# Performance work log

Measured on AMD Instinct MI355X. Metric: run time of the kernel, lower is better.

## Reference

```python
import jax, jax.numpy as jnp
import numpy as np

N = 100000   # nodes
E = 1600000  # edges
G = 64       # graphs in batch
DIMS = [(7, 128), (128, 128), (128, 256)]
EPS = 1e-5


def setup_inputs() -> dict:
    key = jax.random.key(0)
    ks = jax.random.split(key, 32)
    inp = {}
    inp["x"] = jax.random.normal(ks[0], (N, 7), dtype=jnp.float32)
    inp["edge_index"] = jax.random.randint(ks[1], (2, E), 0, N, dtype=jnp.int64)
    inp["batch"] = jnp.sort(jax.random.randint(ks[2], (N,), 0, G, dtype=jnp.int64))
    ki = 3
    for i, (din, dout) in enumerate(DIMS):
        inp[f"Wl{i}"] = jax.random.normal(ks[ki], (din, dout), dtype=jnp.float32) * 0.05; ki += 1
        inp[f"bl{i}"] = jnp.zeros((dout,), dtype=jnp.float32)
        inp[f"Wr{i}"] = jax.random.normal(ks[ki], (din, dout), dtype=jnp.float32) * 0.05; ki += 1
        inp[f"g{i}"] = jax.random.uniform(ks[ki], (dout,), dtype=jnp.float32) + 0.5; ki += 1
        inp[f"be{i}"] = jax.random.normal(ks[ki], (dout,), dtype=jnp.float32) * 0.1; ki += 1
        inp[f"rm{i}"] = jax.random.normal(ks[ki], (dout,), dtype=jnp.float32) * 0.1; ki += 1
        inp[f"rv{i}"] = jax.random.uniform(ks[ki], (dout,), dtype=jnp.float32) + 0.5; ki += 1
    return inp


def _sage(x, src, dst, Wl, bl, Wr):
    # mean-aggregate neighbor features: out[i] = mean_{(j->i)} x[j]
    agg = jax.ops.segment_sum(x[src], dst, num_segments=N)          # [N, din]
    cnt = jax.ops.segment_sum(jnp.ones((src.shape[0],), x.dtype), dst, num_segments=N)
    mean = agg / jnp.maximum(cnt, 1.0)[:, None]
    return x @ Wl + bl + mean @ Wr


def _bn_relu(x, g, be, rm, rv):
    # BatchNorm1d in eval mode (running stats) + ReLU; dropout is a no-op in eval
    return jax.nn.relu((x - rm) * jax.lax.rsqrt(rv + EPS) * g + be)


def reference(x, edge_index, batch,
              Wl0, bl0, Wr0, g0, be0, rm0, rv0,
              Wl1, bl1, Wr1, g1, be1, rm1, rv1,
              Wl2, bl2, Wr2, g2, be2, rm2, rv2):
    src, dst = edge_index[0], edge_index[1]
    layers = [(Wl0, bl0, Wr0, g0, be0, rm0, rv0),
              (Wl1, bl1, Wr1, g1, be1, rm1, rv1),
              (Wl2, bl2, Wr2, g2, be2, rm2, rv2)]
    for Wl, bl, Wr, g, be, rm, rv in layers:
        x = _sage(x, src, dst, Wl, bl, Wr)
        x = _bn_relu(x, g, be, rm, rv)
    pooled = jax.ops.segment_sum(x, batch, num_segments=G)  # global_add_pool
    return (pooled, x)
```

## Files before the change

### kernel.cpp

```cpp
#include <hip/hip_runtime.h>
#include <hip/hip_bf16.h>

#define EPSV 1e-5f
#define PSHIFT 6
#define PMASK 63
#define PCAP 1536
#define B1SHIFT 11
#define B1MASK ((1 << B1SHIFT) - 1)
#define B1CAP 34816
#define SPLIT 16

typedef __attribute__((ext_vector_type(8))) short bf16x8;
typedef __attribute__((ext_vector_type(4))) float f32x4;
typedef __attribute__((ext_vector_type(4))) unsigned u32x4;

__device__ __forceinline__ float bf2f(unsigned short u) {
    unsigned x = ((unsigned)u) << 16;
    return __builtin_bit_cast(float, x);
}
__device__ __forceinline__ unsigned short f2bf(float f) {
    unsigned x = __builtin_bit_cast(unsigned, f);
    unsigned r = (x + 0x7fffu + ((x >> 16) & 1u)) >> 16;
    return (unsigned short)r;
}
__device__ __forceinline__ f32x4 bflo4(u32x4 v) {
    f32x4 r;
    r.x = __builtin_bit_cast(float, v.x << 16);
    r.y = __builtin_bit_cast(float, v.y << 16);
    r.z = __builtin_bit_cast(float, v.z << 16);
    r.w = __builtin_bit_cast(float, v.w << 16);
    return r;
}
__device__ __forceinline__ f32x4 bfhi4(u32x4 v) {
    f32x4 r;
    r.x = __builtin_bit_cast(float, v.x & 0xffff0000u);
    r.y = __builtin_bit_cast(float, v.y & 0xffff0000u);
    r.z = __builtin_bit_cast(float, v.z & 0xffff0000u);
    r.w = __builtin_bit_cast(float, v.w & 0xffff0000u);
    return r;
}


__global__ __launch_bounds__(256) void k_scatter1(const int* __restrict__ src,
                                                  const int* __restrict__ dst,
                                                  int* __restrict__ bcnt1,
                                                  unsigned* __restrict__ stg1,
                                                  int E, int NB1) {
    __shared__ int hist[64], sbase[64], scur[64];
    int t = threadIdx.x;
    int base = blockIdx.x * 2048;
    if (t < 64) { hist[t] = 0; scur[t] = 0; }
    __syncthreads();
    unsigned val[8];
    int cb[8];
#pragma unroll
    for (int k = 0; k < 8; k++) {
        int i = base + k * 256 + t;
        if (i < E) {
            int d = __builtin_nontemporal_load(&dst[i]);
            int s = __builtin_nontemporal_load(&src[i]);
            cb[k] = d >> B1SHIFT;
            val[k] = ((unsigned)s << B1SHIFT) | (unsigned)(d & B1MASK);
            atomicAdd(&hist[cb[k]], 1);
        } else
            cb[k] = -1;
    }
    __syncthreads();
    if (t < NB1 && hist[t] > 0) sbase[t] = atomicAdd(&bcnt1[t], hist[t]);
    __syncthreads();
#pragma unroll
    for (int k = 0; k < 8; k++) {
        if (cb[k] >= 0) {
            int r = atomicAdd(&scur[cb[k]], 1);
            int slot = sbase[cb[k]] + r;
            if (slot < B1CAP) stg1[(size_t)cb[k] * B1CAP + slot] = val[k];
        }
    }
}

__global__ __launch_bounds__(256) void k_scatter2(const int* __restrict__ bcnt1,
                                                  const unsigned* __restrict__ stg1,
                                                  int* __restrict__ pcnt,
                                                  unsigned* __restrict__ pstg) {
    __shared__ int hist[32], sbase[32], scur[32];
    int cb = blockIdx.x >> 4;
    int sl = blockIdx.x & (SPLIT - 1);
    int t = threadIdx.x;
    if (t < 32) { hist[t] = 0; scur[t] = 0; }
    int cnt = min(bcnt1[cb], B1CAP);
    int per = (cnt + SPLIT - 1) / SPLIT;
    int lo = sl * per, hi = min(lo + per, cnt);
    __syncthreads();
    const unsigned* sp = stg1 + (size_t)cb * B1CAP;
    for (int j = lo + t; j < hi; j += 256)
        atomicAdd(&hist[(sp[j] >> 6) & 31], 1);
    __syncthreads();
    if (t < 32 && hist[t] > 0) sbase[t] = atomicAdd(&pcnt[(cb << 5) + t], hist[t]);
    __syncthreads();
    for (int j = lo + t; j < hi; j += 256) {
        unsigned v = sp[j];
        int pr = (v >> 6) & 31;
        int r = atomicAdd(&scur[pr], 1);
        int slot = sbase[pr] + r;
        if (slot < PCAP)
            pstg[(size_t)((cb << 5) + pr) * PCAP + slot] =
                ((v >> 5) & ~63u) | (v & 63u);
    }
}

__global__ __launch_bounds__(256) void k_meta(const int* __restrict__ pcnt,
                                              int* __restrict__ pbase,
                                              int* __restrict__ off,
                                              const int* __restrict__ batch,
                                              int* __restrict__ gstart,
                                              int NPART, int Nn, int G) {
    if (blockIdx.x == 1) {
        int g = threadIdx.x;
        if (g > G) return;
        if (g == G) {
            gstart[G] = Nn;
            return;
        }
        int lo = 0, hi = Nn;
        while (lo < hi) {
            int mid = (lo + hi) >> 1;
            if (batch[mid] < g) lo = mid + 1;
            else hi = mid;
        }
        gstart[g] = lo;
        return;
    }
    __shared__ int red[256];
    int t = threadIdx.x;
    int chunk = (NPART + 255) / 256;
    int lo = t * chunk, hi = min(lo + chunk, NPART);
    int s = 0;
    for (int p = lo; p < hi; p++) {
        int tt = min(pcnt[p], PCAP);
        pbase[p] = tt;
        s += tt;
    }
    red[t] = s;
    __syncthreads();
    for (int d = 1; d < 256; d <<= 1) {
        int v = (t >= d) ? red[t - d] : 0;
        __syncthreads();
        red[t] += v;
        __syncthreads();
    }
    int base = (t == 0) ? 0 : red[t - 1];
    for (int p = lo; p < hi; p++) {
        int tt = pbase[p];
        pbase[p] = base;
        base += tt;
    }
    if (t == 255) off[Nn] = red[255];
}

__global__ __launch_bounds__(256) void k_build(const int* __restrict__ pcnt,
                                               const unsigned* __restrict__ pstg,
                                               const int* __restrict__ pbase,
                                               int* __restrict__ off,
                                               int* __restrict__ csr, int Nn) {
    __shared__ unsigned ed[PCAP];
    __shared__ int srt[PCAP];
    __shared__ int cnt[64], loff[64], cur[64];
    int p = blockIdx.x, t = threadIdx.x;
    int tot = min(pcnt[p], PCAP);
    if (t < 64) cnt[t] = 0;
    __syncthreads();
    const unsigned* sp = pstg + (size_t)p * PCAP;
    for (int j = t; j < tot; j += 256) {
        unsigned e = __builtin_nontemporal_load(&sp[j]);
        ed[j] = e;
        atomicAdd(&cnt[e & PMASK], 1);
    }
    __syncthreads();
    if (t == 0) {
        int a = 0;
        for (int j = 0; j < 64; j++) {
            loff[j] = a;
            cur[j] = a;
            a += cnt[j];
        }
    }
    __syncthreads();
    int base = pbase[p];
    int node0 = p << PSHIFT;
    if (t < 64 && node0 + t < Nn) off[node0 + t] = base + loff[t];
    for (int j = t; j < tot; j += 256) {
        unsigned e = ed[j];
        int pos = atomicAdd(&cur[e & PMASK], 1);
        srt[pos] = (int)(e >> PSHIFT);
    }
    __syncthreads();
    for (int j = t; j < tot; j += 256) csr[base + j] = srt[j];
}


__global__ __launch_bounds__(256) void k_agg7(const float* __restrict__ x,
                                              const int* __restrict__ off,
                                              const int* __restrict__ csr,
                                              float* __restrict__ mean, int n) {
    int i = (blockIdx.x * 256 + threadIdx.x) >> 3;
    int r = threadIdx.x & 7;
    if (i >= n) return;
    int a = off[i], b = off[i + 1];
    float acc = 0.f;
    if (r < 7) {
        int j = a;
        for (; j + 1 < b; j += 2)
            acc += x[(size_t)csr[j] * 7 + r] + x[(size_t)csr[j + 1] * 7 + r];
        if (j < b) acc += x[(size_t)csr[j] * 7 + r];
    }
    float inv = 1.0f / (float)max(b - a, 1);
    if (r < 7) mean[(size_t)i * 7 + r] = acc * inv;
}

__global__ __launch_bounds__(256) void k_agg128(const unsigned short* __restrict__ x,
                                                const int* __restrict__ off,
                                                const int* __restrict__ csr,
                                                unsigned short* __restrict__ mean,
                                                int n) {
    int q = (blockIdx.x * 256 + threadIdx.x) >> 4;
    int sl = threadIdx.x & 15;
    if (q >= n) return;
    int a = off[q], b = off[q + 1];
    const u32x4* xr = (const u32x4*)x;
    f32x4 aL = {0.f, 0.f, 0.f, 0.f}, aH = {0.f, 0.f, 0.f, 0.f};
    int j = a;
    for (; j + 7 < b; j += 8) {
        u32x4 v[8];
#pragma unroll
        for (int t = 0; t < 8; t++) {
            int s = __builtin_nontemporal_load(&csr[j + t]);
            v[t] = xr[(size_t)s * 16 + sl];
        }
#pragma unroll
        for (int t = 0; t < 8; t++) {
            aL += bflo4(v[t]);
            aH += bfhi4(v[t]);
        }
    }
    for (; j + 3 < b; j += 4) {
        u32x4 v[4];
#pragma unroll
        for (int t = 0; t < 4; t++) {
            int s = __builtin_nontemporal_load(&csr[j + t]);
            v[t] = xr[(size_t)s * 16 + sl];
        }
#pragma unroll
        for (int t = 0; t < 4; t++) {
            aL += bflo4(v[t]);
            aH += bfhi4(v[t]);
        }
    }
    for (; j < b; j++) {
        int s = __builtin_nontemporal_load(&csr[j]);
        u32x4 v = xr[(size_t)s * 16 + sl];
        aL += bflo4(v);
        aH += bfhi4(v);
    }
    float inv = 1.0f / (float)max(b - a, 1);
    u32x4 o;
    o.x = (unsigned)f2bf(aL.x * inv) | ((unsigned)f2bf(aH.x * inv) << 16);
    o.y = (unsigned)f2bf(aL.y * inv) | ((unsigned)f2bf(aH.y * inv) << 16);
    o.z = (unsigned)f2bf(aL.z * inv) | ((unsigned)f2bf(aH.z * inv) << 16);
    o.w = (unsigned)f2bf(aL.w * inv) | ((unsigned)f2bf(aH.w * inv) << 16);
    *((u32x4*)mean + (size_t)q * 16 + sl) = o;
}


__global__ __launch_bounds__(256) void k_prepw_all(
    const float* __restrict__ Wl1, const float* __restrict__ Wr1,
    const float* __restrict__ Wl2, const float* __restrict__ Wr2,
    unsigned short* __restrict__ Wlt1, unsigned short* __restrict__ Wrt1,
    unsigned short* __restrict__ Wlt2, unsigned short* __restrict__ Wrt2) {
    int u = blockIdx.x * 256 + threadIdx.x;
    const float* W;
    unsigned short* Wt;
    int Ncols, v;
    if (u < 32768) {
        v = u & 16383;
        W = (u < 16384) ? Wl1 : Wr1;
        Wt = (u < 16384) ? Wlt1 : Wrt1;
        Ncols = 128;
    } else {
        v = (u - 32768) & 32767;
        W = (u < 65536) ? Wl2 : Wr2;
        Wt = (u < 65536) ? Wlt2 : Wrt2;
        Ncols = 256;
    }
    int n = v % Ncols, k = v / Ncols;
    Wt[(size_t)n * 128 + k] = f2bf(W[(size_t)k * Ncols + n]);
}


__global__ __launch_bounds__(256) void k_layer0(
    const float* __restrict__ x, const float* __restrict__ mean,
    const float* __restrict__ Wl, const float* __restrict__ bl,
    const float* __restrict__ Wr, const float* __restrict__ g,
    const float* __restrict__ be, const float* __restrict__ rm,
    const float* __restrict__ rv, unsigned short* __restrict__ out, int n) {
    int tid = threadIdx.x;
    int col = tid & 127;
    int r = tid >> 7;
    int row = blockIdx.x * 2 + r;
    if (row >= n) return;
    float sc = g[col] * rsqrtf(rv[col] + EPSV);
    float sh = (bl[col] - rm[col]) * sc + be[col];
    const float* xp = x + (size_t)row * 7;
    const float* mp = mean + (size_t)row * 7;
    float acc = 0.f;
#pragma unroll
    for (int k = 0; k < 7; k++) acc += xp[k] * Wl[k * 128 + col];
#pragma unroll
    for (int k = 0; k < 7; k++) acc += mp[k] * Wr[k * 128 + col];
    float h = acc * sc + sh;
    out[(size_t)row * 128 + col] = f2bf(fmaxf(h, 0.f));
}


template <int COLS, int DOUT, bool BF16OUT>
__global__ __launch_bounds__(256) void k_mfma_layer(
    const unsigned short* __restrict__ xin, const unsigned short* __restrict__ meanb,
    const unsigned short* __restrict__ Wlt, const unsigned short* __restrict__ Wrt,
    const float* __restrict__ bl, const float* __restrict__ g,
    const float* __restrict__ be, const float* __restrict__ rm,
    const float* __restrict__ rv, void* __restrict__ outv, int n) {
    __shared__ unsigned short As[64 * 40];
    __shared__ unsigned short Bs[COLS * 40];

    int tid = threadIdx.x;
    int wave = tid >> 6;
    int lane = tid & 63;
    int m = lane & 15;
    int half = lane >> 4;
    int row0 = blockIdx.x * 64;
    int colbase = blockIdx.y * COLS;

    const int NCB = COLS / 16;
    f32x4 acc[NCB] = {};

    for (int s = 0; s < 8; s++) {
        int pass = s >> 2;
        int k0 = (s & 3) * 32;
        const unsigned short* Asrc = pass ? meanb : xin;
        const unsigned short* Wt = pass ? Wrt : Wlt;

        __syncthreads();
        {
            int rr = tid >> 2;
            int ks = (tid & 3) * 8;
            int grow = row0 + rr;
            float4 v = make_float4(0.f, 0.f, 0.f, 0.f);
            if (grow < n) v = *(const float4*)&Asrc[(size_t)grow * 128 + k0 + ks];
            *(float4*)&As[rr * 40 + ks] = v;
        }
#pragma unroll
        for (int rep = 0; rep < COLS / 64; rep++) {
            int u = tid + rep * 256;
            int nn = u >> 2;
            int ks = (u & 3) * 8;
            float4 v = *(const float4*)&Wt[(size_t)(colbase + nn) * 128 + k0 + ks];
            *(float4*)&Bs[nn * 40 + ks] = v;
        }
        __syncthreads();

        bf16x8 a = *(const bf16x8*)&As[(wave * 16 + m) * 40 + half * 8];
#pragma unroll
        for (int cb = 0; cb < NCB; cb++) {
            bf16x8 b = *(const bf16x8*)&Bs[(cb * 16 + m) * 40 + half * 8];
            acc[cb] = __builtin_amdgcn_mfma_f32_16x16x32_bf16(a, b, acc[cb], 0, 0, 0);
        }
    }

    float* outf = (float*)outv;
    unsigned short* outb = (unsigned short*)outv;
#pragma unroll
    for (int cb = 0; cb < NCB; cb++) {
        int col = colbase + cb * 16 + m;
        float sc = g[col] * rsqrtf(rv[col] + EPSV);
        float sh = (bl[col] - rm[col]) * sc + be[col];
#pragma unroll
        for (int reg = 0; reg < 4; reg++) {
            int r0 = row0 + wave * 16 + half * 4 + reg;
            if (r0 < n) {
                float h = fmaxf(acc[cb][reg] * sc + sh, 0.f);
                if (BF16OUT) outb[(size_t)r0 * DOUT + col] = f2bf(h);
                else outf[(size_t)r0 * DOUT + col] = h;
            }
        }
    }
}


__global__ __launch_bounds__(256) void k_pool(const float* __restrict__ x3,
                                              const int* __restrict__ gstart,
                                              float* __restrict__ pooled, int G) {
    const int S = 16;
    int g = blockIdx.x / S;
    int s = blockIdx.x % S;
    int a = gstart[g], b = gstart[g + 1];
    int col = threadIdx.x;
    float acc = 0.f;
    for (int r = a + s; r < b; r += S) acc += x3[(size_t)r * 256 + col];
    atomicAdd(&pooled[g * 256 + col], acc);
}


extern "C" void kernel_launch(void* const* d_in, const int* in_sizes, int n_in,
                              void* d_out, int out_size, void* d_ws, size_t ws_size,
                              hipStream_t stream) {
    const float* x = (const float*)d_in[0];
    const int* ei = (const int*)d_in[1];
    const int* batch = (const int*)d_in[2];
    const int N = in_sizes[0] / 7;
    const int E = in_sizes[1] / 2;
    const int G = 64;
    const int* src = ei;
    const int* dst = ei + E;
    const int NPART = (N + PMASK) >> PSHIFT;
    const int NB1 = (N + (1 << B1SHIFT) - 1) >> B1SHIFT;

    const float* P[21];
    for (int i = 0; i < 21; i++) P[i] = (const float*)d_in[3 + i];
    const float **L0 = P, **L1 = P + 7, **L2 = P + 14;

    char* w = (char*)d_ws;
    auto carve = [&](size_t bytes) {
        void* p = (void*)w;
        w += (bytes + 255) & ~(size_t)255;
        return p;
    };
    int* cnts = (int*)carve((size_t)(64 + NPART) * 4);
    int* bcnt1 = cnts;
    int* pcnt = cnts + 64;
    unsigned* stg1 = (unsigned*)carve((size_t)NB1 * B1CAP * 4);
    unsigned* pstg = (unsigned*)carve((size_t)NPART * PCAP * 4);
    int* pbase = (int*)carve((size_t)NPART * 4);
    int* off = (int*)carve(((size_t)N + 1) * 4);
    int* gstart = (int*)carve(((size_t)G + 1) * 4);
    float* mean7 = (float*)carve((size_t)N * 7 * 4);
    unsigned short* x1 = (unsigned short*)carve((size_t)N * 128 * 2);
    unsigned short* meanb = (unsigned short*)carve((size_t)N * 128 * 2);
    unsigned short* Wlt1 = (unsigned short*)carve((size_t)128 * 128 * 2);
    unsigned short* Wrt1 = (unsigned short*)carve((size_t)128 * 128 * 2);
    unsigned short* Wlt2 = (unsigned short*)carve((size_t)128 * 256 * 2);
    unsigned short* Wrt2 = (unsigned short*)carve((size_t)128 * 256 * 2);
    int* csr = (int*)stg1;

    float* pooled = (float*)d_out;
    float* x3 = (float*)d_out + (size_t)G * 256;

    hipMemsetAsync(cnts, 0, (size_t)(64 + NPART) * 4, stream);
    hipMemsetAsync(pooled, 0, (size_t)G * 256 * 4, stream);

    k_scatter1<<<(E + 2047) / 2048, 256, 0, stream>>>(src, dst, bcnt1, stg1, E, NB1);
    k_scatter2<<<NB1 * SPLIT, 256, 0, stream>>>(bcnt1, stg1, pcnt, pstg);
    k_meta<<<2, 256, 0, stream>>>(pcnt, pbase, off, batch, gstart, NPART, N, G);
    k_build<<<NPART, 256, 0, stream>>>(pcnt, pstg, pbase, off, csr, N);
    k_prepw_all<<<(98304 + 255) / 256, 256, 0, stream>>>(L1[0], L1[2], L2[0], L2[2],
                                                         Wlt1, Wrt1, Wlt2, Wrt2);

    k_agg7<<<(N * 8 + 255) / 256, 256, 0, stream>>>(x, off, csr, mean7, N);
    k_layer0<<<(N + 1) / 2, 256, 0, stream>>>(x, mean7, L0[0], L0[1], L0[2], L0[3],
                                              L0[4], L0[5], L0[6], x1, N);

    k_agg128<<<((size_t)N * 16 + 255) / 256, 256, 0, stream>>>(x1, off, csr, meanb, N);
    k_mfma_layer<128, 128, true><<<dim3((N + 63) / 64, 1), 256, 0, stream>>>(
        x1, meanb, Wlt1, Wrt1, L1[1], L1[3], L1[4], L1[5], L1[6], x1, N);

    k_agg128<<<((size_t)N * 16 + 255) / 256, 256, 0, stream>>>(x1, off, csr, meanb, N);
    k_mfma_layer<128, 256, false><<<dim3((N + 63) / 64, 2), 256, 0, stream>>>(
        x1, meanb, Wlt2, Wrt2, L2[1], L2[3], L2[4], L2[5], L2[6], x3, N);

    k_pool<<<G * 16, 256, 0, stream>>>(x3, gstart, pooled, G);
}
```

Baseline: 490.9 us.

## Fuse neighbor mean aggregation into MFMA layer kernels via shared memory

Removes the separate k_agg128 kernels and computes each 64-row tile's neighbor mean directly into shared memory inside the MFMA layer kernel, so the mean matrix is never written to and re-read from global memory. Layer 2 now computes all 256 output columns in a single block instead of splitting across two blocks on grid y, which avoids aggregating twice. The costs are more shared memory per block (lower occupancy), a less unrolled gather loop with fewer loads in flight, and a serial gather phase ahead of the GEMM that limits latency hiding. The output also moves from in-place x1 to a separate x2 buffer.

After: 498.8 us. About the same (+1.6%).

```diff
diff --git a/kernel.cpp b/kernel.cpp
--- a/kernel.cpp
+++ b/kernel.cpp
@@ -215,59 +215,6 @@
     }
     float inv = 1.0f / (float)max(b - a, 1);
     if (r < 7) mean[(size_t)i * 7 + r] = acc * inv;
-}
-
-__global__ __launch_bounds__(256) void k_agg128(const unsigned short* __restrict__ x,
-                                                const int* __restrict__ off,
-                                                const int* __restrict__ csr,
-                                                unsigned short* __restrict__ mean,
-                                                int n) {
-    int q = (blockIdx.x * 256 + threadIdx.x) >> 4;
-    int sl = threadIdx.x & 15;
-    if (q >= n) return;
-    int a = off[q], b = off[q + 1];
-    const u32x4* xr = (const u32x4*)x;
-    f32x4 aL = {0.f, 0.f, 0.f, 0.f}, aH = {0.f, 0.f, 0.f, 0.f};
-    int j = a;
-    for (; j + 7 < b; j += 8) {
-        u32x4 v[8];
-#pragma unroll
-        for (int t = 0; t < 8; t++) {
-            int s = __builtin_nontemporal_load(&csr[j + t]);
-            v[t] = xr[(size_t)s * 16 + sl];
-        }
-#pragma unroll
-        for (int t = 0; t < 8; t++) {
-            aL += bflo4(v[t]);
-            aH += bfhi4(v[t]);
-        }
-    }
-    for (; j + 3 < b; j += 4) {
-        u32x4 v[4];
-#pragma unroll
-        for (int t = 0; t < 4; t++) {
-            int s = __builtin_nontemporal_load(&csr[j + t]);
-            v[t] = xr[(size_t)s * 16 + sl];
-        }
-#pragma unroll
-        for (int t = 0; t < 4; t++) {
-            aL += bflo4(v[t]);
-            aH += bfhi4(v[t]);
-        }
-    }
-    for (; j < b; j++) {
-        int s = __builtin_nontemporal_load(&csr[j]);
-        u32x4 v = xr[(size_t)s * 16 + sl];
-        aL += bflo4(v);
-        aH += bfhi4(v);
-    }
-    float inv = 1.0f / (float)max(b - a, 1);
-    u32x4 o;
-    o.x = (unsigned)f2bf(aL.x * inv) | ((unsigned)f2bf(aH.x * inv) << 16);
-    o.y = (unsigned)f2bf(aL.y * inv) | ((unsigned)f2bf(aH.y * inv) << 16);
-    o.z = (unsigned)f2bf(aL.z * inv) | ((unsigned)f2bf(aH.z * inv) << 16);
-    o.w = (unsigned)f2bf(aL.w * inv) | ((unsigned)f2bf(aH.w * inv) << 16);
-    *((u32x4*)mean + (size_t)q * 16 + sl) = o;
 }
 
 
@@ -321,13 +268,15 @@
 }
 
 
-template <int COLS, int DOUT, bool BF16OUT>
-__global__ __launch_bounds__(256) void k_mfma_layer(
-    const unsigned short* __restrict__ xin, const unsigned short* __restrict__ meanb,
+template <int COLS, bool BF16OUT>
+__global__ __launch_bounds__(256) void k_fused_layer(
+    const unsigned short* __restrict__ xin,
+    const int* __restrict__ off, const int* __restrict__ csr,
     const unsigned short* __restrict__ Wlt, const unsigned short* __restrict__ Wrt,
     const float* __restrict__ bl, const float* __restrict__ g,
     const float* __restrict__ be, const float* __restrict__ rm,
     const float* __restrict__ rv, void* __restrict__ outv, int n) {
+    __shared__ unsigned short Ms[64 * 136];
     __shared__ unsigned short As[64 * 40];
     __shared__ unsigned short Bs[COLS * 40];
 
@@ -337,37 +286,76 @@
     int m = lane & 15;
     int half = lane >> 4;
     int row0 = blockIdx.x * 64;
-    int colbase = blockIdx.y * COLS;
+
+    {
+        int qw = tid >> 4;
+        int sl = tid & 15;
+        const u32x4* xr = (const u32x4*)xin;
+        for (int r4 = 0; r4 < 4; r4++) {
+            int row = qw * 4 + r4;
+            int grow = row0 + row;
+            f32x4 aL = {0.f, 0.f, 0.f, 0.f}, aH = {0.f, 0.f, 0.f, 0.f};
+            float inv = 0.f;
+            if (grow < n) {
+                int a = off[grow], b = off[grow + 1];
+                int j = a;
+                for (; j + 3 < b; j += 4) {
+                    int s0 = csr[j], s1 = csr[j + 1], s2 = csr[j + 2], s3 = csr[j + 3];
+                    u32x4 v0 = xr[(size_t)s0 * 16 + sl];
+                    u32x4 v1 = xr[(size_t)s1 * 16 + sl];
+                    u32x4 v2 = xr[(size_t)s2 * 16 + sl];
+                    u32x4 v3 = xr[(size_t)s3 * 16 + sl];
+                    aL += bflo4(v0) + bflo4(v1) + bflo4(v2) + bflo4(v3);
+                    aH += bfhi4(v0) + bfhi4(v1) + bfhi4(v2) + bfhi4(v3);
+                }
+                for (; j < b; j++) {
+                    u32x4 v = xr[(size_t)csr[j] * 16 + sl];
+                    aL += bflo4(v);
+                    aH += bfhi4(v);
+                }
+                inv = 1.0f / (float)max(b - a, 1);
+            }
+            u32x4 o;
+            o.x = (unsigned)f2bf(aL.x * inv) | ((unsigned)f2bf(aH.x * inv) << 16);
+            o.y = (unsigned)f2bf(aL.y * inv) | ((unsigned)f2bf(aH.y * inv) << 16);
+            o.z = (unsigned)f2bf(aL.z * inv) | ((unsigned)f2bf(aH.z * inv) << 16);
+            o.w = (unsigned)f2bf(aL.w * inv) | ((unsigned)f2bf(aH.w * inv) << 16);
+            *(u32x4*)&Ms[row * 136 + sl * 8] = o;
+        }
+    }
 
     const int NCB = COLS / 16;
     f32x4 acc[NCB] = {};
+    int rr = tid >> 2;
+    int ks = (tid & 3) * 8;
 
     for (int s = 0; s < 8; s++) {
         int pass = s >> 2;
         int k0 = (s & 3) * 32;
-        const unsigned short* Asrc = pass ? meanb : xin;
         const unsigned short* Wt = pass ? Wrt : Wlt;
 
         __syncthreads();
-        {
-            int rr = tid >> 2;
-            int ks = (tid & 3) * 8;
+        if (pass == 0) {
             int grow = row0 + rr;
             float4 v = make_float4(0.f, 0.f, 0.f, 0.f);
-            if (grow < n) v = *(const float4*)&Asrc[(size_t)grow * 128 + k0 + ks];
+            if (grow < n) v = *(const float4*)&xin[(size_t)grow * 128 + k0 + ks];
             *(float4*)&As[rr * 40 + ks] = v;
         }
 #pragma unroll
         for (int rep = 0; rep < COLS / 64; rep++) {
             int u = tid + rep * 256;
             int nn = u >> 2;
-            int ks = (u & 3) * 8;
-            float4 v = *(const float4*)&Wt[(size_t)(colbase + nn) * 128 + k0 + ks];
-            *(float4*)&Bs[nn * 40 + ks] = v;
+            int ks2 = (u & 3) * 8;
+            float4 v = *(const float4*)&Wt[(size_t)nn * 128 + k0 + ks2];
+            *(float4*)&Bs[nn * 40 + ks2] = v;
         }
         __syncthreads();
 
-        bf16x8 a = *(const bf16x8*)&As[(wave * 16 + m) * 40 + half * 8];
+        bf16x8 a;
+        if (pass == 0)
+            a = *(const bf16x8*)&As[(wave * 16 + m) * 40 + half * 8];
+        else
+            a = *(const bf16x8*)&Ms[(wave * 16 + m) * 136 + k0 + half * 8];
 #pragma unroll
         for (int cb = 0; cb < NCB; cb++) {
             bf16x8 b = *(const bf16x8*)&Bs[(cb * 16 + m) * 40 + half * 8];
@@ -379,7 +367,7 @@
     unsigned short* outb = (unsigned short*)outv;
 #pragma unroll
     for (int cb = 0; cb < NCB; cb++) {
-        int col = colbase + cb * 16 + m;
+        int col = cb * 16 + m;
         float sc = g[col] * rsqrtf(rv[col] + EPSV);
         float sh = (bl[col] - rm[col]) * sc + be[col];
 #pragma unroll
@@ -387,8 +375,8 @@
             int r0 = row0 + wave * 16 + half * 4 + reg;
             if (r0 < n) {
                 float h = fmaxf(acc[cb][reg] * sc + sh, 0.f);
-                if (BF16OUT) outb[(size_t)r0 * DOUT + col] = f2bf(h);
-                else outf[(size_t)r0 * DOUT + col] = h;
+                if (BF16OUT) outb[(size_t)r0 * COLS + col] = f2bf(h);
+                else outf[(size_t)r0 * COLS + col] = h;
             }
         }
     }
@@ -443,7 +431,7 @@
     int* gstart = (int*)carve(((size_t)G + 1) * 4);
     float* mean7 = (float*)carve((size_t)N * 7 * 4);
     unsigned short* x1 = (unsigned short*)carve((size_t)N * 128 * 2);
-    unsigned short* meanb = (unsigned short*)carve((size_t)N * 128 * 2);
+    unsigned short* x2 = (unsigned short*)carve((size_t)N * 128 * 2);
     unsigned short* Wlt1 = (unsigned short*)carve((size_t)128 * 128 * 2);
     unsigned short* Wrt1 = (unsigned short*)carve((size_t)128 * 128 * 2);
     unsigned short* Wlt2 = (unsigned short*)carve((size_t)128 * 256 * 2);
@@ -467,13 +455,11 @@
     k_layer0<<<(N + 1) / 2, 256, 0, stream>>>(x, mean7, L0[0], L0[1], L0[2], L0[3],
                                               L0[4], L0[5], L0[6], x1, N);
 
-    k_agg128<<<((size_t)N * 16 + 255) / 256, 256, 0, stream>>>(x1, off, csr, meanb, N);
-    k_mfma_layer<128, 128, true><<<dim3((N + 63) / 64, 1), 256, 0, stream>>>(
-        x1, meanb, Wlt1, Wrt1, L1[1], L1[3], L1[4], L1[5], L1[6], x1, N);
-
-    k_agg128<<<((size_t)N * 16 + 255) / 256, 256, 0, stream>>>(x1, off, csr, meanb, N);
-    k_mfma_layer<128, 256, false><<<dim3((N + 63) / 64, 2), 256, 0, stream>>>(
-        x1, meanb, Wlt2, Wrt2, L2[1], L2[3], L2[4], L2[5], L2[6], x3, N);
+    k_fused_layer<128, true><<<(N + 63) / 64, 256, 0, stream>>>(
+        x1, off, csr, Wlt1, Wrt1, L1[1], L1[3], L1[4], L1[5], L1[6], x2, N);
+
+    k_fused_layer<256, false><<<(N + 63) / 64, 256, 0, stream>>>(
+        x2, off, csr, Wlt2, Wrt2, L2[1], L2[3], L2[4], L2[5], L2[6], x3, N);
 
     k_pool<<<G * 16, 256, 0, stream>>>(x3, gstart, pooled, G);
 }
```
